# Kernel optimization log

Measured on AMD Instinct MI355X. Metric: run time of the kernel, lower is better.

## Reference

```python
import jax, jax.numpy as jnp
import numpy as np

D_MODEL = 512
NHEAD = 8
HEAD_DIM = D_MODEL // NHEAD  # 64, also rotary_dim
WIN_LO, WIN_HI = 127, 128    # attn_window: kv in [q-127, q+128]
BLOCK = 256                  # block size for banded attention (>= WIN_LO+1 and >= WIN_HI)


def setup_inputs() -> dict:
    key = jax.random.key(0)
    k1, k2, k3, k4 = jax.random.split(key, 4)
    N, T = 4, 2048
    x = jax.random.normal(k1, (N, T, D_MODEL), dtype=jnp.float32)
    Wqkv_w = jax.random.normal(k2, (3 * D_MODEL, D_MODEL), dtype=jnp.float32) * 0.02
    out_w = jax.random.normal(k3, (D_MODEL, D_MODEL), dtype=jnp.float32) * 0.02
    out_b = jax.random.normal(k4, (D_MODEL,), dtype=jnp.float32) * 0.02
    return {"x": x, "Wqkv_w": Wqkv_w, "out_w": out_w, "out_b": out_b}


def _rotate_half(u):
    u1, u2 = jnp.split(u, 2, axis=-1)
    return jnp.concatenate((-u2, u1), axis=-1)


def _apply_rope(q, k, T, dtype):
    # inv_freq: [HEAD_DIM/2]
    inv_freq = 1.0 / (10000.0 ** (jnp.arange(0, HEAD_DIM, 2, dtype=jnp.float32) / HEAD_DIM))
    pos = jnp.arange(T, dtype=dtype)
    freqs = pos[:, None] * inv_freq[None, :].astype(dtype)      # [T, D/2]
    emb = jnp.concatenate((freqs, freqs), axis=-1)              # [T, D]
    cos = jnp.cos(emb)[None, :, None, :]                        # [1,T,1,D]
    sin = jnp.sin(emb)[None, :, None, :]
    q = q * cos + _rotate_half(q) * sin
    k = k * cos + _rotate_half(k) * sin
    return q, k


def reference(x, Wqkv_w, out_w, out_b):
    N, T, dm = x.shape
    H, D, B = NHEAD, HEAD_DIM, BLOCK
    qkv = (x @ Wqkv_w.T).reshape(N, T, 3, H, D)
    q, k, v = qkv[:, :, 0], qkv[:, :, 1], qkv[:, :, 2]          # [N,T,H,D]
    q, k = _apply_rope(q, k, T, x.dtype)
    # [N,H,T,D]
    q = q.transpose(0, 2, 1, 3)
    k = k.transpose(0, 2, 1, 3)
    v = v.transpose(0, 2, 1, 3)

    nb = T // B
    qb = q.reshape(N, H, nb, B, D)
    kb = k.reshape(N, H, nb, B, D)
    vb = v.reshape(N, H, nb, B, D)
    # pad one block of zeros on each side so block g sees key blocks g-1,g,g+1
    pad = ((0, 0), (0, 0), (1, 1), (0, 0), (0, 0))
    kp = jnp.pad(kb, pad)
    vp = jnp.pad(vb, pad)
    # [N,H,nb,3B,D]
    kwin = jnp.concatenate([kp[:, :, i:i + nb] for i in range(3)], axis=3)
    vwin = jnp.concatenate([vp[:, :, i:i + nb] for i in range(3)], axis=3)

    scale = 1.0 / np.sqrt(D)
    scores = jnp.einsum('nhgqd,nhgkd->nhgqk', qb, kwin) * scale  # [N,H,nb,B,3B]

    qi = jnp.arange(B)
    kj = jnp.arange(3 * B)
    gidx = jnp.arange(nb)
    diff = kj[None, None, :] - B - qi[None, :, None]             # [1,B,3B] kv - q offset
    band = (diff >= -WIN_LO) & (diff <= WIN_HI)
    kv_global = gidx[:, None, None] * B + kj[None, None, :] - B  # [nb,1,3B]
    valid = (kv_global >= 0) & (kv_global < T)
    mask = band & valid                                          # [nb,B,3B]

    neg = jnp.asarray(-1e30, dtype=scores.dtype)
    scores = jnp.where(mask[None, None], scores, neg)
    probs = jax.nn.softmax(scores, axis=-1)
    attn = jnp.einsum('nhgqk,nhgkd->nhgqd', probs, vwin)         # [N,H,nb,B,D]
    attn = attn.reshape(N, H, T, D).transpose(0, 2, 1, 3).reshape(N, T, dm)
    return attn @ out_w.T + out_b
```

## Files before the change

kernel.cpp:

```cpp
#include <hip/hip_runtime.h>
#include <math.h>


typedef __attribute__((ext_vector_type(8))) __bf16 bf16x8;
typedef __attribute__((ext_vector_type(4))) float f32x4;

__device__ __forceinline__ unsigned short f2bf(float f) {
    unsigned int u = __float_as_uint(f);
    u += 0x7fffu + ((u >> 16) & 1u);
    return (unsigned short)(u >> 16);
}
__device__ __forceinline__ unsigned int packbf2(float a, float b) {
    unsigned int ua = __float_as_uint(a); ua += 0x7fffu + ((ua >> 16) & 1u);
    unsigned int ub = __float_as_uint(b); ub += 0x7fffu + ((ub >> 16) & 1u);
    return (ua >> 16) | (ub & 0xffff0000u);
}
__device__ __forceinline__ bf16x8 as_bf16x8(uint4 u) {
    union { uint4 u4; bf16x8 v; } c; c.u4 = u; return c.v;
}
__device__ __forceinline__ bf16x8 ld_frag(const unsigned short* p) {
    return as_bf16x8(*(const uint4*)p);
}

__device__ __forceinline__ void async16(void* lds, const void* g) {
    __builtin_amdgcn_global_load_lds(
        (const __attribute__((address_space(1))) void*)g,
        (__attribute__((address_space(3))) void*)lds,
        16, 0, 0);
}

__global__ __launch_bounds__(256) void cvt_all(
    const float* __restrict__ x, const float* __restrict__ w1,
    const float* __restrict__ w2,
    unsigned short* __restrict__ xb, unsigned short* __restrict__ w1b,
    unsigned short* __restrict__ w2b)
{
    const int n_x  = 8192 * 512 / 4;
    const int n_w1 = 1536 * 512 / 4;
    const int n_w2 = 512 * 512 / 4;
    int i = blockIdx.x * 256 + threadIdx.x;
    const float* in; unsigned short* out; int j;
    if (i < n_x)                    { in = x;  out = xb;  j = i; }
    else if (i < n_x + n_w1)        { in = w1; out = w1b; j = i - n_x; }
    else if (i < n_x + n_w1 + n_w2) { in = w2; out = w2b; j = i - n_x - n_w1; }
    else return;
    float4 v = *(const float4*)(in + 4 * (size_t)j);
    uint2 o;
    o.x = packbf2(v.x, v.y);
    o.y = packbf2(v.z, v.w);
    *(uint2*)(out + 4 * (size_t)j) = o;
}

__global__ __launch_bounds__(256, 5) void gemm_bt_mfma(
    const unsigned short* __restrict__ A, const unsigned short* __restrict__ B,
    const float* __restrict__ bias, void* __restrict__ Cout,
    int M, int O, int K, int write_bf16, int do_rope)
{
    __shared__ __align__(16) unsigned short As[128 * 64];
    __shared__ __align__(16) unsigned short Bs[64 * 64];

    const int tid  = threadIdx.x;
    const int wave = tid >> 6;
    const int lane = tid & 63;
    const int l15  = lane & 15;
    const int lg   = lane >> 4;
    const int row0 = blockIdx.x * 128;
    const int col0 = blockIdx.y * 64;
    const int wr   = wave * 32;

    f32x4 acc[2][4] = {};

    const int srow = tid >> 3;
    const int skg  = ((tid & 7) * 8) ^ ((srow & 7) * 8);
    const int fx   = (l15 & 7) * 8;

    for (int k0 = 0; k0 < K; k0 += 64) {
        #pragma unroll
        for (int s = 0; s < 4; ++s)
            async16(&As[(size_t)(s * 256 + tid) * 8],
                    A + (size_t)(row0 + s * 32 + srow) * K + k0 + skg);
        #pragma unroll
        for (int s = 0; s < 2; ++s)
            async16(&Bs[(size_t)(s * 256 + tid) * 8],
                    B + (size_t)(col0 + s * 32 + srow) * K + k0 + skg);
        __syncthreads();

        #pragma unroll
        for (int kstep = 0; kstep < 2; ++kstep) {
            const int kq = (kstep * 32 + lg * 8) ^ fx;
            bf16x8 af[2], bfr[4];
            #pragma unroll
            for (int mt = 0; mt < 2; ++mt)
                af[mt] = ld_frag(&As[(wr + mt * 16 + l15) * 64 + kq]);
            #pragma unroll
            for (int nt = 0; nt < 4; ++nt)
                bfr[nt] = ld_frag(&Bs[(nt * 16 + l15) * 64 + kq]);
            #pragma unroll
            for (int mt = 0; mt < 2; ++mt)
                #pragma unroll
                for (int nt = 0; nt < 4; ++nt)
                    acc[mt][nt] = __builtin_amdgcn_mfma_f32_16x16x32_bf16(
                        af[mt], bfr[nt], acc[mt][nt], 0, 0, 0);
        }
        __syncthreads();
    }

    const int qrow = lg * 4;

    if (do_rope && col0 < 1024) {
        const float cfreq = 0.28782313662425574f;
        const float invf0 = __expf(-(float)l15 * cfreq);
        const float invf1 = __expf(-(float)(16 + l15) * cfreq);
        #pragma unroll
        for (int mt = 0; mt < 2; ++mt) {
            #pragma unroll
            for (int r = 0; r < 4; ++r) {
                const int t = (row0 + wr + mt * 16 + qrow + r) & 2047;
                #pragma unroll
                for (int p = 0; p < 2; ++p) {
                    float ang = (float)t * (p ? invf1 : invf0);
                    float s, c;
                    __sincosf(ang, &s, &c);
                    float a = acc[mt][p][r];
                    float b = acc[mt][p + 2][r];
                    acc[mt][p][r]     = a * c - b * s;
                    acc[mt][p + 2][r] = b * c + a * s;
                }
            }
        }
        if (col0 < 512) {
            #pragma unroll
            for (int mt = 0; mt < 2; ++mt)
                #pragma unroll
                for (int nt = 0; nt < 4; ++nt)
                    #pragma unroll
                    for (int r = 0; r < 4; ++r)
                        acc[mt][nt][r] *= 0.125f;
        }
    }

    #pragma unroll
    for (int nt = 0; nt < 4; ++nt) {
        const int col = col0 + nt * 16 + l15;
        const float bv = bias ? bias[col] : 0.f;
        #pragma unroll
        for (int mt = 0; mt < 2; ++mt) {
            const int rowb = row0 + wr + mt * 16 + qrow;
            if (write_bf16) {
                unsigned short* C = (unsigned short*)Cout;
                #pragma unroll
                for (int r = 0; r < 4; ++r)
                    C[(size_t)(rowb + r) * O + col] = f2bf(acc[mt][nt][r] + bv);
            } else {
                float* C = (float*)Cout;
                #pragma unroll
                for (int r = 0; r < 4; ++r)
                    C[(size_t)(rowb + r) * O + col] = acc[mt][nt][r] + bv;
            }
        }
    }
}

__global__ __launch_bounds__(256) void attn_mfma_kernel(
    const unsigned short* __restrict__ qkv, unsigned short* __restrict__ attnout)
{
    __shared__ __align__(16) unsigned short Kt[64 * 72];
    __shared__ __align__(16) unsigned short Vt[64 * 72];
    __shared__ __align__(16) unsigned short Ps[4][16 * 72];

    const int qt = blockIdx.x;
    const int h  = blockIdx.y;
    const int n  = blockIdx.z;
    const int t0 = qt * 64;
    const int tid  = threadIdx.x;
    const int wave = tid >> 6;
    const int lane = tid & 63;
    const int l15  = lane & 15;
    const int lg   = lane >> 4;

    const size_t base = (size_t)n * 2048 * 1536 + (size_t)h * 64;

    bf16x8 qfrag[2];
    {
        const unsigned short* qp = qkv + base + (size_t)(t0 + wave * 16 + l15) * 1536;
        qfrag[0] = ld_frag(qp + lg * 8);
        qfrag[1] = ld_frag(qp + 32 + lg * 8);
    }

    const int skey = tid >> 2;
    const int sd0  = (tid & 3) * 16;

    float m_r[4], l_r[4];
    #pragma unroll
    for (int r = 0; r < 4; ++r) { m_r[r] = -1e30f; l_r[r] = 0.f; }
    f32x4 acc_o[4] = {};

    for (int dt = -2; dt <= 2; ++dt) {
        const int kt = qt + dt;
        if (kt < 0 || kt > 31) continue;
        const int s0 = kt * 64;

        {
            const unsigned short* kp = qkv + base + 512 + (size_t)(s0 + skey) * 1536 + sd0;
            uint4 k0 = *(const uint4*)kp;
            uint4 k1 = *(const uint4*)(kp + 8);
            *(uint4*)&Kt[skey * 72 + sd0]     = k0;
            *(uint4*)&Kt[skey * 72 + sd0 + 8] = k1;

            const unsigned short* vp = qkv + base + 1024 + (size_t)(s0 + skey) * 1536 + sd0;
            uint4 a = *(const uint4*)vp;
            uint4 b = *(const uint4*)(vp + 8);
            Vt[(sd0 +  0) * 72 + skey] = (unsigned short)(a.x & 0xffffu);
            Vt[(sd0 +  1) * 72 + skey] = (unsigned short)(a.x >> 16);
            Vt[(sd0 +  2) * 72 + skey] = (unsigned short)(a.y & 0xffffu);
            Vt[(sd0 +  3) * 72 + skey] = (unsigned short)(a.y >> 16);
            Vt[(sd0 +  4) * 72 + skey] = (unsigned short)(a.z & 0xffffu);
            Vt[(sd0 +  5) * 72 + skey] = (unsigned short)(a.z >> 16);
            Vt[(sd0 +  6) * 72 + skey] = (unsigned short)(a.w & 0xffffu);
            Vt[(sd0 +  7) * 72 + skey] = (unsigned short)(a.w >> 16);
            Vt[(sd0 +  8) * 72 + skey] = (unsigned short)(b.x & 0xffffu);
            Vt[(sd0 +  9) * 72 + skey] = (unsigned short)(b.x >> 16);
            Vt[(sd0 + 10) * 72 + skey] = (unsigned short)(b.y & 0xffffu);
            Vt[(sd0 + 11) * 72 + skey] = (unsigned short)(b.y >> 16);
            Vt[(sd0 + 12) * 72 + skey] = (unsigned short)(b.z & 0xffffu);
            Vt[(sd0 + 13) * 72 + skey] = (unsigned short)(b.z >> 16);
            Vt[(sd0 + 14) * 72 + skey] = (unsigned short)(b.w & 0xffffu);
            Vt[(sd0 + 15) * 72 + skey] = (unsigned short)(b.w >> 16);
        }
        __syncthreads();

        f32x4 acc_s[4] = {};
        #pragma unroll
        for (int kstep = 0; kstep < 2; ++kstep) {
            #pragma unroll
            for (int nt = 0; nt < 4; ++nt) {
                if ((dt == -2 && nt < wave) || (dt == 2 && nt > wave)) continue;
                bf16x8 kf = ld_frag(&Kt[(nt * 16 + l15) * 72 + kstep * 32 + lg * 8]);
                acc_s[nt] = __builtin_amdgcn_mfma_f32_16x16x32_bf16(
                    qfrag[kstep], kf, acc_s[nt], 0, 0, 0);
            }
        }

        float sc[4][4];
        #pragma unroll
        for (int nt = 0; nt < 4; ++nt) {
            const int key_off = dt * 64 + nt * 16 + l15;
            #pragma unroll
            for (int r = 0; r < 4; ++r) {
                const int diff = key_off - (wave * 16 + lg * 4 + r);
                const bool ok = (diff >= -127) && (diff <= 128);
                sc[nt][r] = ok ? acc_s[nt][r] : -1e30f;
            }
        }
        #pragma unroll
        for (int r = 0; r < 4; ++r) {
            float tm = fmaxf(fmaxf(sc[0][r], sc[1][r]), fmaxf(sc[2][r], sc[3][r]));
            tm = fmaxf(tm, __shfl_xor(tm, 1, 64));
            tm = fmaxf(tm, __shfl_xor(tm, 2, 64));
            tm = fmaxf(tm, __shfl_xor(tm, 4, 64));
            tm = fmaxf(tm, __shfl_xor(tm, 8, 64));
            const float m_new = fmaxf(m_r[r], tm);
            const float alpha = __expf(m_r[r] - m_new);
            float psum = 0.f;
            #pragma unroll
            for (int nt = 0; nt < 4; ++nt) {
                float p = __expf(sc[nt][r] - m_new);
                sc[nt][r] = p;
                psum += p;
            }
            psum += __shfl_xor(psum, 1, 64);
            psum += __shfl_xor(psum, 2, 64);
            psum += __shfl_xor(psum, 4, 64);
            psum += __shfl_xor(psum, 8, 64);
            l_r[r] = l_r[r] * alpha + psum;
            m_r[r] = m_new;
            #pragma unroll
            for (int nt = 0; nt < 4; ++nt) acc_o[nt][r] *= alpha;
        }

        #pragma unroll
        for (int nt = 0; nt < 4; ++nt)
            #pragma unroll
            for (int r = 0; r < 4; ++r)
                Ps[wave][(lg * 4 + r) * 72 + nt * 16 + l15] = f2bf(sc[nt][r]);

        __syncthreads();

        bf16x8 pfrag[2];
        pfrag[0] = ld_frag(&Ps[wave][l15 * 72 + lg * 8]);
        pfrag[1] = ld_frag(&Ps[wave][l15 * 72 + 32 + lg * 8]);

        #pragma unroll
        for (int kstep = 0; kstep < 2; ++kstep) {
            #pragma unroll
            for (int nt = 0; nt < 4; ++nt) {
                bf16x8 vf = ld_frag(&Vt[(nt * 16 + l15) * 72 + kstep * 32 + lg * 8]);
                acc_o[nt] = __builtin_amdgcn_mfma_f32_16x16x32_bf16(
                    pfrag[kstep], vf, acc_o[nt], 0, 0, 0);
            }
        }
        __syncthreads();
    }

    float inv_l[4];
    #pragma unroll
    for (int r = 0; r < 4; ++r) inv_l[r] = 1.0f / l_r[r];

    #pragma unroll
    for (int r = 0; r < 4; ++r) {
        const int tq = t0 + wave * 16 + lg * 4 + r;
        unsigned short* op = attnout + (size_t)(n * 2048 + tq) * 512 + h * 64;
        #pragma unroll
        for (int nt = 0; nt < 4; ++nt)
            op[nt * 16 + l15] = f2bf(acc_o[nt][r] * inv_l[r]);
    }
}

extern "C" void kernel_launch(void* const* d_in, const int* in_sizes, int n_in,
                              void* d_out, int out_size, void* d_ws, size_t ws_size,
                              hipStream_t stream)
{
    (void)in_sizes; (void)n_in; (void)out_size; (void)ws_size;

    const float* x     = (const float*)d_in[0];
    const float* Wqkv  = (const float*)d_in[1];
    const float* out_w = (const float*)d_in[2];
    const float* out_b = (const float*)d_in[3];
    float* out = (float*)d_out;

    unsigned short* qkvb  = (unsigned short*)d_ws;
    unsigned short* attnb = qkvb + (size_t)8192 * 1536;
    unsigned short* xb    = attnb + (size_t)8192 * 512;
    unsigned short* wqkvb = xb + (size_t)8192 * 512;
    unsigned short* outwb = wqkvb + (size_t)1536 * 512;

    cvt_all<<<5120, 256, 0, stream>>>(x, Wqkv, out_w, xb, wqkvb, outwb);

    gemm_bt_mfma<<<dim3(64, 24), 256, 0, stream>>>(xb, wqkvb, nullptr, qkvb,
                                                   8192, 1536, 512, 1, 1);
    attn_mfma_kernel<<<dim3(32, 8, 4), 256, 0, stream>>>(qkvb, attnb);
    gemm_bt_mfma<<<dim3(64, 8), 256, 0, stream>>>(attnb, outwb, out_b, out,
                                                  8192, 512, 512, 0, 0);
}
```

Before: 134.5 us.

## Write V transposed from QKV GEMM epilogue to avoid LDS transpose in attention

The QKV projection GEMM now writes the V third of its output directly in a per-head transposed [n,h,d,t] bf16 layout into a new workspace buffer. The attention kernel then loads V tiles with vectorized 16-byte loads and stores, replacing the per-element scattered 2-byte LDS writes that did the transpose before. The cost is strided 8-byte global stores in the GEMM epilogue and extra workspace memory.

```diff
diff --git a/kernel.cpp b/kernel.cpp
--- a/kernel.cpp
+++ b/kernel.cpp
@@ -54,7 +54,8 @@
 __global__ __launch_bounds__(256, 5) void gemm_bt_mfma(
     const unsigned short* __restrict__ A, const unsigned short* __restrict__ B,
     const float* __restrict__ bias, void* __restrict__ Cout,
-    int M, int O, int K, int write_bf16, int do_rope)
+    int M, int O, int K, int write_bf16, int do_rope,
+    unsigned short* __restrict__ vT)
 {
     __shared__ __align__(16) unsigned short As[128 * 64];
     __shared__ __align__(16) unsigned short Bs[64 * 64];
@@ -139,6 +140,26 @@
         }
     }
 
+    if (do_rope && col0 >= 1024) {
+        #pragma unroll
+        for (int nt = 0; nt < 4; ++nt) {
+            const int local = col0 - 1024 + nt * 16 + l15;
+            const int hh = local >> 6;
+            const int dd = local & 63;
+            #pragma unroll
+            for (int mt = 0; mt < 2; ++mt) {
+                const int rowb = row0 + wr + mt * 16 + qrow;
+                const int nn = rowb >> 11;
+                const int tt = rowb & 2047;
+                uint2 o;
+                o.x = packbf2(acc[mt][nt][0], acc[mt][nt][1]);
+                o.y = packbf2(acc[mt][nt][2], acc[mt][nt][3]);
+                *(uint2*)(vT + ((size_t)(nn * 8 + hh) * 64 + dd) * 2048 + tt) = o;
+            }
+        }
+        return;
+    }
+
     #pragma unroll
     for (int nt = 0; nt < 4; ++nt) {
         const int col = col0 + nt * 16 + l15;
@@ -162,7 +183,9 @@
 }
 
 __global__ __launch_bounds__(256) void attn_mfma_kernel(
-    const unsigned short* __restrict__ qkv, unsigned short* __restrict__ attnout)
+    const unsigned short* __restrict__ qkv,
+    const unsigned short* __restrict__ vT,
+    unsigned short* __restrict__ attnout)
 {
     __shared__ __align__(16) unsigned short Kt[64 * 72];
     __shared__ __align__(16) unsigned short Vt[64 * 72];
@@ -179,6 +202,7 @@
     const int lg   = lane >> 4;
 
     const size_t base = (size_t)n * 2048 * 1536 + (size_t)h * 64;
+    const unsigned short* vTh = vT + (size_t)(n * 8 + h) * 64 * 2048;
 
     bf16x8 qfrag[2];
     {
@@ -202,30 +226,12 @@
 
         {
             const unsigned short* kp = qkv + base + 512 + (size_t)(s0 + skey) * 1536 + sd0;
-            uint4 k0 = *(const uint4*)kp;
-            uint4 k1 = *(const uint4*)(kp + 8);
-            *(uint4*)&Kt[skey * 72 + sd0]     = k0;
-            *(uint4*)&Kt[skey * 72 + sd0 + 8] = k1;
-
-            const unsigned short* vp = qkv + base + 1024 + (size_t)(s0 + skey) * 1536 + sd0;
-            uint4 a = *(const uint4*)vp;
-            uint4 b = *(const uint4*)(vp + 8);
-            Vt[(sd0 +  0) * 72 + skey] = (unsigned short)(a.x & 0xffffu);
-            Vt[(sd0 +  1) * 72 + skey] = (unsigned short)(a.x >> 16);
-            Vt[(sd0 +  2) * 72 + skey] = (unsigned short)(a.y & 0xffffu);
-            Vt[(sd0 +  3) * 72 + skey] = (unsigned short)(a.y >> 16);
-            Vt[(sd0 +  4) * 72 + skey] = (unsigned short)(a.z & 0xffffu);
-            Vt[(sd0 +  5) * 72 + skey] = (unsigned short)(a.z >> 16);
-            Vt[(sd0 +  6) * 72 + skey] = (unsigned short)(a.w & 0xffffu);
-            Vt[(sd0 +  7) * 72 + skey] = (unsigned short)(a.w >> 16);
-            Vt[(sd0 +  8) * 72 + skey] = (unsigned short)(b.x & 0xffffu);
-            Vt[(sd0 +  9) * 72 + skey] = (unsigned short)(b.x >> 16);
-            Vt[(sd0 + 10) * 72 + skey] = (unsigned short)(b.y & 0xffffu);
-            Vt[(sd0 + 11) * 72 + skey] = (unsigned short)(b.y >> 16);
-            Vt[(sd0 + 12) * 72 + skey] = (unsigned short)(b.z & 0xffffu);
-            Vt[(sd0 + 13) * 72 + skey] = (unsigned short)(b.z >> 16);
-            Vt[(sd0 + 14) * 72 + skey] = (unsigned short)(b.w & 0xffffu);
-            Vt[(sd0 + 15) * 72 + skey] = (unsigned short)(b.w >> 16);
+            *(uint4*)&Kt[skey * 72 + sd0]     = *(const uint4*)kp;
+            *(uint4*)&Kt[skey * 72 + sd0 + 8] = *(const uint4*)(kp + 8);
+
+            const unsigned short* vp = vTh + (size_t)skey * 2048 + s0 + sd0;
+            *(uint4*)&Vt[skey * 72 + sd0]     = *(const uint4*)vp;
+            *(uint4*)&Vt[skey * 72 + sd0 + 8] = *(const uint4*)(vp + 8);
         }
         __syncthreads();
 
@@ -333,12 +339,13 @@
     unsigned short* xb    = attnb + (size_t)8192 * 512;
     unsigned short* wqkvb = xb + (size_t)8192 * 512;
     unsigned short* outwb = wqkvb + (size_t)1536 * 512;
+    unsigned short* vTb   = outwb + (size_t)512 * 512;
 
     cvt_all<<<5120, 256, 0, stream>>>(x, Wqkv, out_w, xb, wqkvb, outwb);
 
     gemm_bt_mfma<<<dim3(64, 24), 256, 0, stream>>>(xb, wqkvb, nullptr, qkvb,
-                                                   8192, 1536, 512, 1, 1);
-    attn_mfma_kernel<<<dim3(32, 8, 4), 256, 0, stream>>>(qkvb, attnb);
+                                                   8192, 1536, 512, 1, 1, vTb);
+    attn_mfma_kernel<<<dim3(32, 8, 4), 256, 0, stream>>>(qkvb, vTb, attnb);
     gemm_bt_mfma<<<dim3(64, 8), 256, 0, stream>>>(attnb, outwb, out_b, out,
-                                                  8192, 512, 512, 0, 0);
-}
+                                                  8192, 512, 512, 0, 0, nullptr);
+}
```

New measurement: 130.3 us. 3.1% less time.
